# Kernel optimization log

Hardware: AMD Instinct MI355X
Metric: run time of the kernel (lower is better)

The kernel has to match this reference:

```python
import jax, jax.numpy as jnp
import numpy as np
import math

D_MODEL, D_K, N_HEADS = 1024, 64, 16
N, T = 2, 2048


def setup_inputs() -> dict:
    key = jax.random.key(0)
    ks = jax.random.split(key, 12)
    s = 1.0 / math.sqrt(D_MODEL)
    dh = D_K * N_HEADS
    return {
        "k": jax.random.normal(ks[0], (N, T, D_MODEL), jnp.float32),
        "q": jax.random.normal(ks[1], (N, T, D_MODEL), jnp.float32),
        "v": jax.random.normal(ks[2], (N, T, D_MODEL), jnp.float32),
        "mask": jnp.ones((N, T), jnp.int32),
        "Wk": jax.random.normal(ks[3], (D_MODEL, dh), jnp.float32) * s,
        "bk": jnp.zeros((dh,), jnp.float32),
        "Wq": jax.random.normal(ks[4], (D_MODEL, dh), jnp.float32) * s,
        "bq": jnp.zeros((dh,), jnp.float32),
        "Wv": jax.random.normal(ks[5], (D_MODEL, dh), jnp.float32) * s,
        "bv": jnp.zeros((dh,), jnp.float32),
        "Wo": jax.random.normal(ks[6], (dh, D_MODEL), jnp.float32) * (1.0 / math.sqrt(dh)),
        "bo": jnp.zeros((D_MODEL,), jnp.float32),
    }


def reference(k, q, v, mask, Wk, bk, Wq, bq, Wv, bv, Wo, bo):
    n, t = k.shape[0], k.shape[1]
    # project and split heads -> (N, H, T, d_k)
    K = (k @ Wk + bk).reshape(n, t, N_HEADS, D_K).transpose(0, 2, 1, 3)
    Q = (q @ Wq + bq).reshape(n, t, N_HEADS, D_K).transpose(0, 2, 1, 3)
    V = (v @ Wv + bv).reshape(n, t, N_HEADS, D_K).transpose(0, 2, 1, 3)
    scores = jnp.einsum("bhqd,bhkd->bhqk", Q, K) / math.sqrt(D_K)
    scores = jnp.where(mask[:, None, None, :] == 0, -jnp.inf, scores)
    weights = jax.nn.softmax(scores, axis=-1)
    A = jnp.einsum("bhqk,bhkd->bhqd", weights, V)
    A = A.transpose(0, 2, 1, 3).reshape(n, t, N_HEADS * D_K)
    return A @ Wo + bo
```

## Files before the change

### kernel.cpp

```cpp
#include <hip/hip_runtime.h>


typedef __bf16 bf16;
typedef __bf16 bf16x8 __attribute__((ext_vector_type(8)));
typedef __bf16 bf16x4 __attribute__((ext_vector_type(4)));
typedef float f32x4 __attribute__((ext_vector_type(4)));

#define MFMA16(a, b, c) __builtin_amdgcn_mfma_f32_16x16x32_bf16((a), (b), (c), 0, 0, 0)
#define EXP2(x) __builtin_amdgcn_exp2f(x)

__device__ __forceinline__ void load_lds16(const bf16* g, bf16* l) {
  __builtin_amdgcn_global_load_lds(
      (const __attribute__((address_space(1))) unsigned int*)g,
      (__attribute__((address_space(3))) unsigned int*)l, 16, 0, 0);
}

__device__ __forceinline__ bf16x8 cvt8(const float* __restrict__ p) {
  const f32x4 a = *(const f32x4*)p;
  const f32x4 b = *(const f32x4*)(p + 4);
  bf16x8 r;
  r[0] = (bf16)a[0]; r[1] = (bf16)a[1]; r[2] = (bf16)a[2]; r[3] = (bf16)a[3];
  r[4] = (bf16)b[0]; r[5] = (bf16)b[1]; r[6] = (bf16)b[2]; r[7] = (bf16)b[3];
  return r;
}

__global__ __launch_bounds__(256) void prep(
    const float* __restrict__ ka, const float* __restrict__ qa,
    const float* __restrict__ va, bf16* __restrict__ kb,
    bf16* __restrict__ qb, bf16* __restrict__ vb,
    const float* __restrict__ W0, const float* __restrict__ W1,
    const float* __restrict__ W2, const float* __restrict__ W3,
    bf16* __restrict__ T0, bf16* __restrict__ T1, bf16* __restrict__ T2,
    bf16* __restrict__ T3, const int* __restrict__ mask,
    unsigned long long* __restrict__ mbits) {
  __shared__ bf16 t[64 * 72];
  const int tid = threadIdx.x;
  if (blockIdx.x < 6144) {
    const size_t i = ((size_t)blockIdx.x * 256 + tid) * 8;
    const int which = (int)(i >> 22);
    const size_t off = i & ((size_t)(1u << 22) - 1);
    const float* src = which == 0 ? ka : (which == 1 ? qa : va);
    bf16* dst = which == 0 ? kb : (which == 1 ? qb : vb);
    *(bf16x8*)&dst[off] = cvt8(&src[off]);
    return;
  }
  const int tb = blockIdx.x - 6144;
  const int z = tb >> 8;
  const int rem = tb & 255;
  const int by = rem >> 4, bx = rem & 15;
  const float* W = z == 0 ? W0 : (z == 1 ? W1 : (z == 2 ? W2 : W3));
  bf16* T = z == 0 ? T0 : (z == 1 ? T1 : (z == 2 ? T2 : T3));
  const int kBase = by * 64, nBase = bx * 64;
  const int row = tid >> 2, cs = (tid & 3) * 16;

  const float* src = &W[(size_t)(kBase + row) * 1024 + nBase + cs];
  *(bf16x8*)&t[row * 72 + cs] = cvt8(src);
  *(bf16x8*)&t[row * 72 + cs + 8] = cvt8(src + 8);
  __syncthreads();

  const int n = tid >> 2, ks = (tid & 3) * 16;
  bf16 buf[16];
#pragma unroll
  for (int j = 0; j < 16; ++j) buf[j] = t[(ks + j) * 72 + n];
  bf16* dst = &T[(size_t)(nBase + n) * 1024 + kBase + ks];
  *(bf16x8*)&dst[0] = *(bf16x8*)&buf[0];
  *(bf16x8*)&dst[8] = *(bf16x8*)&buf[8];

  if (bx == 0 && by == 0 && tid < 128) {
    const int w = tid >> 6, lane = tid & 63;
#pragma unroll
    for (int i = 0; i < 8; ++i) {
      const int tile = z * 16 + w * 8 + i;
      const unsigned long long bits = __ballot(mask[tile * 64 + lane] != 0);
      if (lane == 0) mbits[tile] = bits;
    }
  }
}

__global__ __launch_bounds__(256) void gemm_qkv(
    const bf16* __restrict__ kb, const bf16* __restrict__ vb,
    const bf16* __restrict__ qb, const bf16* __restrict__ WkT,
    const bf16* __restrict__ WvT, const bf16* __restrict__ WqT,
    const float* __restrict__ bk, const float* __restrict__ bv,
    const float* __restrict__ bq, bf16* __restrict__ K_buf,
    bf16* __restrict__ Vt_buf, bf16* __restrict__ Q_buf) {
  __shared__ __align__(16) bf16 S[12288];
  bf16* As = S;
  bf16* Ws = S + 8192;
  const int tid = threadIdx.x;
  const int lane = tid & 63, w = tid >> 6;
  const int l15 = lane & 15, quad = lane >> 4;
  const int z = blockIdx.z;
  const bf16* X = z == 0 ? kb : (z == 1 ? vb : qb);
  const bf16* WT = z == 0 ? WkT : (z == 1 ? WvT : WqT);
  const float* B = z == 0 ? bk : (z == 1 ? bv : bq);
  const int mBase = blockIdx.y * 128, nBase = blockIdx.x * 64;
  const int wm = (w >> 1) * 64, wn = (w & 1) * 32;

  const int r8 = tid >> 3;
  const int jg = ((tid & 7) ^ (r8 & 7)) * 8;
  const int sw = l15 & 7;

  f32x4 acc[4][2] = {};

  for (int k0 = 0; k0 < 1024; k0 += 64) {
    __syncthreads();
#pragma unroll
    for (int i = 0; i < 4; ++i)
      load_lds16(&X[(size_t)(mBase + r8 + i * 32) * 1024 + k0 + jg],
                 &As[(tid + i * 256) * 8]);
#pragma unroll
    for (int i = 0; i < 2; ++i)
      load_lds16(&WT[(size_t)(nBase + r8 + i * 32) * 1024 + k0 + jg],
                 &Ws[(tid + i * 256) * 8]);
    __syncthreads();

#pragma unroll
    for (int k2 = 0; k2 < 2; ++k2) {
      const int col = ((k2 * 4 + quad) ^ sw) * 8;
      bf16x8 a[4], bb[2];
#pragma unroll
      for (int mt = 0; mt < 4; ++mt)
        a[mt] = *(const bf16x8*)&As[(wm + mt * 16 + l15) * 64 + col];
#pragma unroll
      for (int nt = 0; nt < 2; ++nt)
        bb[nt] = *(const bf16x8*)&Ws[(wn + nt * 16 + l15) * 64 + col];
#pragma unroll
      for (int mt = 0; mt < 4; ++mt)
#pragma unroll
        for (int nt = 0; nt < 2; ++nt)
          acc[mt][nt] = MFMA16(a[mt], bb[nt], acc[mt][nt]);
    }
  }

  const int h = nBase >> 6;
  if (z != 1) {
    const float scale = (z == 2) ? 0.18033688011112042f : 1.0f;
    bf16* o = (z == 0) ? K_buf : Q_buf;
#pragma unroll
    for (int nt = 0; nt < 2; ++nt) {
      const int n = nBase + wn + nt * 16 + l15;
      const float bias = B[n];
      const int d = n & 63;
#pragma unroll
      for (int mt = 0; mt < 4; ++mt)
#pragma unroll
        for (int r = 0; r < 4; ++r) {
          const int m = mBase + wm + mt * 16 + quad * 4 + r;
          const int b = m >> 11, t = m & 2047;
          o[((size_t)(b * 16 + h) * 2048 + t) * 64 + d] =
              (bf16)((acc[mt][nt][r] + bias) * scale);
        }
    }
  } else {
    __syncthreads();
    bf16* Tb = &S[w * 2304];
#pragma unroll
    for (int nt = 0; nt < 2; ++nt) {
      const int n = nBase + wn + nt * 16 + l15;
      const float bias = B[n];
#pragma unroll
      for (int mt = 0; mt < 4; ++mt) {
        bf16x4 pk;
#pragma unroll
        for (int r = 0; r < 4; ++r) pk[r] = (bf16)(acc[mt][nt][r] + bias);
        *(bf16x4*)&Tb[(nt * 16 + l15) * 72 + mt * 16 + quad * 4] = pk;
      }
    }
    const int b = mBase >> 11;
#pragma unroll
    for (int i = 0; i < 4; ++i) {
      const int dl = i * 8 + (lane >> 3), ts = (lane & 7) * 8;
      const bf16x8 vv = *(const bf16x8*)&Tb[dl * 72 + ts];
      const int d = wn + dl;
      const int t = (mBase + wm + ts) & 2047;
      *(bf16x8*)&Vt_buf[((size_t)(b * 16 + h) * 64 + d) * 2048 + t] = vv;
    }
  }
}

__global__ __launch_bounds__(256) void gemm_out(const bf16* __restrict__ X,
                                                const bf16* __restrict__ WT,
                                                const float* __restrict__ B,
                                                float* __restrict__ out) {
  __shared__ __align__(16) bf16 As[128 * 64];
  __shared__ __align__(16) bf16 Ws[64 * 64];
  const int tid = threadIdx.x;
  const int lane = tid & 63, w = tid >> 6;
  const int l15 = lane & 15, quad = lane >> 4;
  const int mBase = blockIdx.y * 128, nBase = blockIdx.x * 64;
  const int wm = (w >> 1) * 64, wn = (w & 1) * 32;

  const int r8 = tid >> 3;
  const int jg = ((tid & 7) ^ (r8 & 7)) * 8;
  const int sw = l15 & 7;

  f32x4 acc[4][2] = {};

  for (int k0 = 0; k0 < 1024; k0 += 64) {
    __syncthreads();
#pragma unroll
    for (int i = 0; i < 4; ++i)
      load_lds16(&X[(size_t)(mBase + r8 + i * 32) * 1024 + k0 + jg],
                 &As[(tid + i * 256) * 8]);
#pragma unroll
    for (int i = 0; i < 2; ++i)
      load_lds16(&WT[(size_t)(nBase + r8 + i * 32) * 1024 + k0 + jg],
                 &Ws[(tid + i * 256) * 8]);
    __syncthreads();

#pragma unroll
    for (int k2 = 0; k2 < 2; ++k2) {
      const int col = ((k2 * 4 + quad) ^ sw) * 8;
      bf16x8 a[4], bb[2];
#pragma unroll
      for (int mt = 0; mt < 4; ++mt)
        a[mt] = *(const bf16x8*)&As[(wm + mt * 16 + l15) * 64 + col];
#pragma unroll
      for (int nt = 0; nt < 2; ++nt)
        bb[nt] = *(const bf16x8*)&Ws[(wn + nt * 16 + l15) * 64 + col];
#pragma unroll
      for (int mt = 0; mt < 4; ++mt)
#pragma unroll
        for (int nt = 0; nt < 2; ++nt)
          acc[mt][nt] = MFMA16(a[mt], bb[nt], acc[mt][nt]);
    }
  }

#pragma unroll
  for (int nt = 0; nt < 2; ++nt) {
    const int n = nBase + wn + nt * 16 + l15;
    const float bias = B[n];
#pragma unroll
    for (int mt = 0; mt < 4; ++mt)
#pragma unroll
      for (int r = 0; r < 4; ++r) {
        const int m = mBase + wm + mt * 16 + quad * 4 + r;
        out[(size_t)m * 1024 + n] = acc[mt][nt][r] + bias;
      }
  }
}

__global__ __launch_bounds__(256) void flash_attn(
    const bf16* __restrict__ Q, const bf16* __restrict__ K,
    const bf16* __restrict__ Vt, const unsigned long long* __restrict__ mbits,
    bf16* __restrict__ A) {
  __shared__ __align__(16) bf16 Ks[2][64 * 64];
  __shared__ __align__(16) bf16 Vs[64 * 64];
  __shared__ __align__(16) bf16 Ps[128 * 72];

  const int tid = threadIdx.x;
  const int lane = tid & 63, w = tid >> 6;
  const int l15 = lane & 15, quad = lane >> 4;
  const int bh = blockIdx.y;
  const int b = bh >> 4, h = bh & 15;
  const int qt = blockIdx.x * 128;

  const int r8 = tid >> 3;
  const int jg = ((tid & 7) ^ (r8 & 7)) * 8;
  const int sw = l15 & 7;

  const size_t qbaseA = ((size_t)bh * 2048 + qt + w * 32 + l15) * 64;
  const size_t qbaseB = qbaseA + (size_t)16 * 64;
  const bf16x8 qA0 = *(const bf16x8*)&Q[qbaseA + quad * 8];
  const bf16x8 qA1 = *(const bf16x8*)&Q[qbaseA + 32 + quad * 8];
  const bf16x8 qB0 = *(const bf16x8*)&Q[qbaseB + quad * 8];
  const bf16x8 qB1 = *(const bf16x8*)&Q[qbaseB + 32 + quad * 8];

  f32x4 oA[4] = {}, oB[4] = {};
  float rsA = 0.0f, rsB = 0.0f;

  const int rowA = (w * 32 + l15) * 72;
  const int rowB = (w * 32 + 16 + l15) * 72;

#pragma unroll
  for (int i = 0; i < 2; ++i)
    load_lds16(&K[((size_t)bh * 2048 + r8 + i * 32) * 64 + jg],
               &Ks[0][(tid + i * 256) * 8]);

  int cur = 0;
  for (int kt = 0; kt < 2048; kt += 64) {
    __builtin_amdgcn_s_barrier();

    const unsigned long long mb = mbits[b * 32 + (kt >> 6)];

#pragma unroll
    for (int i = 0; i < 2; ++i)
      load_lds16(&Vt[((size_t)bh * 64 + r8 + i * 32) * 2048 + kt + jg],
                 &Vs[(tid + i * 256) * 8]);
    const int ktn = (kt + 64) & 2047;
#pragma unroll
    for (int i = 0; i < 2; ++i)
      load_lds16(&K[((size_t)bh * 2048 + ktn + r8 + i * 32) * 64 + jg],
                 &Ks[cur ^ 1][(tid + i * 256) * 8]);

    asm volatile("s_waitcnt vmcnt(4)" ::: "memory");
    __builtin_amdgcn_s_barrier();

    const bf16* Kc = Ks[cur];
    f32x4 sA[4], sB[4];
    __builtin_amdgcn_s_setprio(1);
#pragma unroll
    for (int nt = 0; nt < 4; ++nt) {
      const bf16x8 ak0 = *(const bf16x8*)&Kc[(nt * 16 + l15) * 64 + ((quad ^ sw) * 8)];
      const bf16x8 ak1 = *(const bf16x8*)&Kc[(nt * 16 + l15) * 64 + (((4 + quad) ^ sw) * 8)];
      f32x4 s = {};
      s = MFMA16(ak0, qA0, s);
      s = MFMA16(ak1, qA1, s);
      sA[nt] = s;
      f32x4 t = {};
      t = MFMA16(ak0, qB0, t);
      t = MFMA16(ak1, qB1, t);
      sB[nt] = t;
    }
    __builtin_amdgcn_s_setprio(0);

    asm volatile("s_waitcnt vmcnt(2)" ::: "memory");

    if (mb + 1ull == 0ull) {
#pragma unroll
      for (int nt = 0; nt < 4; ++nt) {
        const float a0 = EXP2(sA[nt][0]), a1 = EXP2(sA[nt][1]);
        const float a2 = EXP2(sA[nt][2]), a3 = EXP2(sA[nt][3]);
        rsA += (a0 + a1) + (a2 + a3);
        bf16x4 pa;
        pa[0] = (bf16)a0; pa[1] = (bf16)a1; pa[2] = (bf16)a2; pa[3] = (bf16)a3;
        *(bf16x4*)&Ps[rowA + nt * 16 + quad * 4] = pa;
        const float b0 = EXP2(sB[nt][0]), b1 = EXP2(sB[nt][1]);
        const float b2 = EXP2(sB[nt][2]), b3 = EXP2(sB[nt][3]);
        rsB += (b0 + b1) + (b2 + b3);
        bf16x4 pb;
        pb[0] = (bf16)b0; pb[1] = (bf16)b1; pb[2] = (bf16)b2; pb[3] = (bf16)b3;
        *(bf16x4*)&Ps[rowB + nt * 16 + quad * 4] = pb;
      }
    } else {
#pragma unroll
      for (int nt = 0; nt < 4; ++nt) {
        const unsigned g = (unsigned)(mb >> (nt * 16)) & 0xffffu;
        const int bp = quad * 4;
        const unsigned m0 = (g >> (bp + 0)) & 1u, m1 = (g >> (bp + 1)) & 1u;
        const unsigned m2 = (g >> (bp + 2)) & 1u, m3 = (g >> (bp + 3)) & 1u;
        const float a0 = m0 ? EXP2(sA[nt][0]) : 0.0f;
        const float a1 = m1 ? EXP2(sA[nt][1]) : 0.0f;
        const float a2 = m2 ? EXP2(sA[nt][2]) : 0.0f;
        const float a3 = m3 ? EXP2(sA[nt][3]) : 0.0f;
        rsA += (a0 + a1) + (a2 + a3);
        bf16x4 pa;
        pa[0] = (bf16)a0; pa[1] = (bf16)a1; pa[2] = (bf16)a2; pa[3] = (bf16)a3;
        *(bf16x4*)&Ps[rowA + nt * 16 + quad * 4] = pa;
        const float b0 = m0 ? EXP2(sB[nt][0]) : 0.0f;
        const float b1 = m1 ? EXP2(sB[nt][1]) : 0.0f;
        const float b2 = m2 ? EXP2(sB[nt][2]) : 0.0f;
        const float b3 = m3 ? EXP2(sB[nt][3]) : 0.0f;
        rsB += (b0 + b1) + (b2 + b3);
        bf16x4 pb;
        pb[0] = (bf16)b0; pb[1] = (bf16)b1; pb[2] = (bf16)b2; pb[3] = (bf16)b3;
        *(bf16x4*)&Ps[rowB + nt * 16 + quad * 4] = pb;
      }
    }

    __builtin_amdgcn_s_barrier();

    __builtin_amdgcn_s_setprio(1);
#pragma unroll
    for (int ks = 0; ks < 2; ++ks) {
      const bf16x8 bpA = *(const bf16x8*)&Ps[rowA + ks * 32 + quad * 8];
      const bf16x8 bpB = *(const bf16x8*)&Ps[rowB + ks * 32 + quad * 8];
#pragma unroll
      for (int mt = 0; mt < 4; ++mt) {
        const bf16x8 av =
            *(const bf16x8*)&Vs[(mt * 16 + l15) * 64 + (((ks * 4 + quad) ^ sw) * 8)];
        oA[mt] = MFMA16(av, bpA, oA[mt]);
        oB[mt] = MFMA16(av, bpB, oB[mt]);
      }
    }
    __builtin_amdgcn_s_setprio(0);

    cur ^= 1;
  }

  rsA += __shfl_xor(rsA, 16);
  rsA += __shfl_xor(rsA, 32);
  rsB += __shfl_xor(rsB, 16);
  rsB += __shfl_xor(rsB, 32);
  const float invA = rsA > 0.0f ? 1.0f / rsA : 0.0f;
  const float invB = rsB > 0.0f ? 1.0f / rsB : 0.0f;

  const int tA = qt + w * 32 + l15;
  const size_t baseA = ((size_t)b * 2048 + tA) * 1024 + h * 64;
  const size_t baseB = baseA + (size_t)16 * 1024;
#pragma unroll
  for (int mt = 0; mt < 4; ++mt) {
    bf16x4 ovA, ovB;
#pragma unroll
    for (int r = 0; r < 4; ++r) {
      ovA[r] = (bf16)(oA[mt][r] * invA);
      ovB[r] = (bf16)(oB[mt][r] * invB);
    }
    *(bf16x4*)&A[baseA + mt * 16 + quad * 4] = ovA;
    *(bf16x4*)&A[baseB + mt * 16 + quad * 4] = ovB;
  }
}

extern "C" void kernel_launch(void* const* d_in, const int* in_sizes, int n_in,
                              void* d_out, int out_size, void* d_ws, size_t ws_size,
                              hipStream_t stream) {
  const float* k = (const float*)d_in[0];
  const float* q = (const float*)d_in[1];
  const float* v = (const float*)d_in[2];
  const int* mask = (const int*)d_in[3];
  const float* Wk = (const float*)d_in[4];
  const float* bk = (const float*)d_in[5];
  const float* Wq = (const float*)d_in[6];
  const float* bq = (const float*)d_in[7];
  const float* Wv = (const float*)d_in[8];
  const float* bv = (const float*)d_in[9];
  const float* Wo = (const float*)d_in[10];
  const float* bo = (const float*)d_in[11];

  const size_t ELEMS = (size_t)4 * 1024 * 1024;
  const size_t WELEMS = (size_t)1024 * 1024;

  bf16* kb = (bf16*)d_ws;
  bf16* qb = kb + ELEMS;
  bf16* vb = qb + ELEMS;
  bf16* WkT = vb + ELEMS;
  bf16* WqT = WkT + WELEMS;
  bf16* WvT = WqT + WELEMS;
  bf16* WoT = WvT + WELEMS;

  bf16 *K_buf, *Q_buf, *Vt_buf, *A_buf;
  if (ws_size >= ((size_t)56 << 20)) {
    bf16* ext = WoT + WELEMS;
    K_buf = ext;
    Q_buf = ext + ELEMS;
    Vt_buf = ext + 2 * ELEMS;
    A_buf = kb;
  } else {
    K_buf = (bf16*)d_in[0];
    Q_buf = (bf16*)d_in[0] + ELEMS;
    Vt_buf = (bf16*)d_in[2];
    A_buf = (bf16*)d_in[2] + ELEMS;
  }
  unsigned long long* mbits = (unsigned long long*)d_out;

  prep<<<7168, 256, 0, stream>>>(k, q, v, kb, qb, vb,
                                 Wk, Wq, Wv, Wo, WkT, WqT, WvT, WoT,
                                 mask, mbits);
  gemm_qkv<<<dim3(16, 32, 3), 256, 0, stream>>>(kb, vb, qb, WkT, WvT, WqT,
                                                bk, bv, bq, K_buf, Vt_buf, Q_buf);
  flash_attn<<<dim3(16, 32), 256, 0, stream>>>(Q_buf, K_buf, Vt_buf, mbits, A_buf);
  gemm_out<<<dim3(16, 32), 256, 0, stream>>>(A_buf, WoT, bo, (float*)d_out);
}
```

Before: 224.7 us.

## Switch attention to 32x32 MFMA and keep P in registers via permlane swap

Rewrites the flash attention inner loop to use 32x32x16 bf16 MFMA tiles for both QK^T and PV. Softmax probabilities are packed with v_cvt_pk_bf16_f32 and rearranged across lane halves with v_permlane32_swap, so they feed the PV MFMA directly instead of going through an LDS round-trip. This drops the Ps shared buffer and its stores and loads, lowers LDS use, and halves the row-sum shuffle work. The cost is more accumulator registers per lane and reliance on gfx950-specific permlane instructions.

After: 243.3 us. 1.08x slower.

```diff
diff --git a/kernel.cpp b/kernel.cpp
--- a/kernel.cpp
+++ b/kernel.cpp
@@ -5,8 +5,11 @@
 typedef __bf16 bf16x8 __attribute__((ext_vector_type(8)));
 typedef __bf16 bf16x4 __attribute__((ext_vector_type(4)));
 typedef float f32x4 __attribute__((ext_vector_type(4)));
+typedef float f32x16 __attribute__((ext_vector_type(16)));
+typedef unsigned u32x4 __attribute__((ext_vector_type(4)));
 
 #define MFMA16(a, b, c) __builtin_amdgcn_mfma_f32_16x16x32_bf16((a), (b), (c), 0, 0, 0)
+#define MFMA32(a, b, c) __builtin_amdgcn_mfma_f32_32x32x16_bf16((a), (b), (c), 0, 0, 0)
 #define EXP2(x) __builtin_amdgcn_exp2f(x)
 
 __device__ __forceinline__ void load_lds16(const bf16* g, bf16* l) {
@@ -247,31 +250,27 @@
     bf16* __restrict__ A) {
   __shared__ __align__(16) bf16 Ks[2][64 * 64];
   __shared__ __align__(16) bf16 Vs[64 * 64];
-  __shared__ __align__(16) bf16 Ps[128 * 72];
 
   const int tid = threadIdx.x;
   const int lane = tid & 63, w = tid >> 6;
-  const int l15 = lane & 15, quad = lane >> 4;
+  const int l31 = lane & 31, hi = lane >> 5;
+  const int m7 = l31 & 7;
   const int bh = blockIdx.y;
   const int b = bh >> 4, h = bh & 15;
   const int qt = blockIdx.x * 128;
 
   const int r8 = tid >> 3;
   const int jg = ((tid & 7) ^ (r8 & 7)) * 8;
-  const int sw = l15 & 7;
-
-  const size_t qbaseA = ((size_t)bh * 2048 + qt + w * 32 + l15) * 64;
-  const size_t qbaseB = qbaseA + (size_t)16 * 64;
-  const bf16x8 qA0 = *(const bf16x8*)&Q[qbaseA + quad * 8];
-  const bf16x8 qA1 = *(const bf16x8*)&Q[qbaseA + 32 + quad * 8];
-  const bf16x8 qB0 = *(const bf16x8*)&Q[qbaseB + quad * 8];
-  const bf16x8 qB1 = *(const bf16x8*)&Q[qbaseB + 32 + quad * 8];
-
-  f32x4 oA[4] = {}, oB[4] = {};
-  float rsA = 0.0f, rsB = 0.0f;
-
-  const int rowA = (w * 32 + l15) * 72;
-  const int rowB = (w * 32 + 16 + l15) * 72;
+
+  const int q = qt + w * 32 + l31;
+  const size_t qbase = ((size_t)bh * 2048 + q) * 64;
+  bf16x8 qf[4];
+#pragma unroll
+  for (int t = 0; t < 4; ++t)
+    qf[t] = *(const bf16x8*)&Q[qbase + t * 16 + hi * 8];
+
+  f32x16 o_acc[2] = {};
+  float rs = 0.0f;
 
 #pragma unroll
   for (int i = 0; i < 2; ++i)
@@ -298,108 +297,100 @@
     __builtin_amdgcn_s_barrier();
 
     const bf16* Kc = Ks[cur];
-    f32x4 sA[4], sB[4];
+    f32x16 s_acc[2];
     __builtin_amdgcn_s_setprio(1);
 #pragma unroll
-    for (int nt = 0; nt < 4; ++nt) {
-      const bf16x8 ak0 = *(const bf16x8*)&Kc[(nt * 16 + l15) * 64 + ((quad ^ sw) * 8)];
-      const bf16x8 ak1 = *(const bf16x8*)&Kc[(nt * 16 + l15) * 64 + (((4 + quad) ^ sw) * 8)];
-      f32x4 s = {};
-      s = MFMA16(ak0, qA0, s);
-      s = MFMA16(ak1, qA1, s);
-      sA[nt] = s;
-      f32x4 t = {};
-      t = MFMA16(ak0, qB0, t);
-      t = MFMA16(ak1, qB1, t);
-      sB[nt] = t;
+    for (int kk = 0; kk < 2; ++kk) {
+      f32x16 s = {};
+#pragma unroll
+      for (int t = 0; t < 4; ++t) {
+        const int row = kk * 32 + l31;
+        const bf16x8 ak =
+            *(const bf16x8*)&Kc[row * 64 + (((2 * t + hi) ^ m7) * 8)];
+        s = MFMA32(ak, qf[t], s);
+      }
+      s_acc[kk] = s;
     }
     __builtin_amdgcn_s_setprio(0);
 
     asm volatile("s_waitcnt vmcnt(2)" ::: "memory");
 
+    unsigned c[2][4][2];
     if (mb + 1ull == 0ull) {
 #pragma unroll
-      for (int nt = 0; nt < 4; ++nt) {
-        const float a0 = EXP2(sA[nt][0]), a1 = EXP2(sA[nt][1]);
-        const float a2 = EXP2(sA[nt][2]), a3 = EXP2(sA[nt][3]);
-        rsA += (a0 + a1) + (a2 + a3);
-        bf16x4 pa;
-        pa[0] = (bf16)a0; pa[1] = (bf16)a1; pa[2] = (bf16)a2; pa[3] = (bf16)a3;
-        *(bf16x4*)&Ps[rowA + nt * 16 + quad * 4] = pa;
-        const float b0 = EXP2(sB[nt][0]), b1 = EXP2(sB[nt][1]);
-        const float b2 = EXP2(sB[nt][2]), b3 = EXP2(sB[nt][3]);
-        rsB += (b0 + b1) + (b2 + b3);
-        bf16x4 pb;
-        pb[0] = (bf16)b0; pb[1] = (bf16)b1; pb[2] = (bf16)b2; pb[3] = (bf16)b3;
-        *(bf16x4*)&Ps[rowB + nt * 16 + quad * 4] = pb;
+      for (int kk = 0; kk < 2; ++kk)
+#pragma unroll
+        for (int sg = 0; sg < 4; ++sg)
+#pragma unroll
+          for (int i = 0; i < 2; ++i) {
+            const float p0 = EXP2(s_acc[kk][sg * 4 + 2 * i]);
+            const float p1 = EXP2(s_acc[kk][sg * 4 + 2 * i + 1]);
+            rs += p0 + p1;
+            unsigned u;
+            asm("v_cvt_pk_bf16_f32 %0, %1, %2" : "=v"(u) : "v"(p0), "v"(p1));
+            c[kk][sg][i] = u;
+          }
+    } else {
+#pragma unroll
+      for (int kk = 0; kk < 2; ++kk) {
+        const unsigned g = (unsigned)(mb >> (kk * 32));
+#pragma unroll
+        for (int sg = 0; sg < 4; ++sg)
+#pragma unroll
+          for (int i = 0; i < 2; ++i) {
+            const int kl = sg * 8 + hi * 4 + 2 * i;
+            const float p0 = ((g >> kl) & 1u) ? EXP2(s_acc[kk][sg * 4 + 2 * i]) : 0.0f;
+            const float p1 = ((g >> (kl + 1)) & 1u) ? EXP2(s_acc[kk][sg * 4 + 2 * i + 1]) : 0.0f;
+            rs += p0 + p1;
+            unsigned u;
+            asm("v_cvt_pk_bf16_f32 %0, %1, %2" : "=v"(u) : "v"(p0), "v"(p1));
+            c[kk][sg][i] = u;
+          }
       }
-    } else {
-#pragma unroll
-      for (int nt = 0; nt < 4; ++nt) {
-        const unsigned g = (unsigned)(mb >> (nt * 16)) & 0xffffu;
-        const int bp = quad * 4;
-        const unsigned m0 = (g >> (bp + 0)) & 1u, m1 = (g >> (bp + 1)) & 1u;
-        const unsigned m2 = (g >> (bp + 2)) & 1u, m3 = (g >> (bp + 3)) & 1u;
-        const float a0 = m0 ? EXP2(sA[nt][0]) : 0.0f;
-        const float a1 = m1 ? EXP2(sA[nt][1]) : 0.0f;
-        const float a2 = m2 ? EXP2(sA[nt][2]) : 0.0f;
-        const float a3 = m3 ? EXP2(sA[nt][3]) : 0.0f;
-        rsA += (a0 + a1) + (a2 + a3);
-        bf16x4 pa;
-        pa[0] = (bf16)a0; pa[1] = (bf16)a1; pa[2] = (bf16)a2; pa[3] = (bf16)a3;
-        *(bf16x4*)&Ps[rowA + nt * 16 + quad * 4] = pa;
-        const float b0 = m0 ? EXP2(sB[nt][0]) : 0.0f;
-        const float b1 = m1 ? EXP2(sB[nt][1]) : 0.0f;
-        const float b2 = m2 ? EXP2(sB[nt][2]) : 0.0f;
-        const float b3 = m3 ? EXP2(sB[nt][3]) : 0.0f;
-        rsB += (b0 + b1) + (b2 + b3);
-        bf16x4 pb;
-        pb[0] = (bf16)b0; pb[1] = (bf16)b1; pb[2] = (bf16)b2; pb[3] = (bf16)b3;
-        *(bf16x4*)&Ps[rowB + nt * 16 + quad * 4] = pb;
+    }
+
+    __builtin_amdgcn_s_barrier();
+
+    const bf16* Vc = Vs;
+    __builtin_amdgcn_s_setprio(1);
+#pragma unroll
+    for (int kk = 0; kk < 2; ++kk)
+#pragma unroll
+      for (int t2 = 0; t2 < 2; ++t2) {
+        unsigned a0 = c[kk][2 * t2][0], b0 = c[kk][2 * t2 + 1][0];
+        asm("v_permlane32_swap_b32 %0, %1" : "+v"(a0), "+v"(b0));
+        unsigned a1 = c[kk][2 * t2][1], b1 = c[kk][2 * t2 + 1][1];
+        asm("v_permlane32_swap_b32 %0, %1" : "+v"(a1), "+v"(b1));
+        u32x4 wv;
+        wv[0] = a0; wv[1] = a1; wv[2] = b0; wv[3] = b1;
+        const bf16x8 bp = __builtin_bit_cast(bf16x8, wv);
+        const int seg = kk * 2 + t2;
+#pragma unroll
+        for (int dt = 0; dt < 2; ++dt) {
+          const int row = dt * 32 + l31;
+          const bf16x8 av =
+              *(const bf16x8*)&Vc[row * 64 + (((seg * 2 + hi) ^ m7) * 8)];
+          o_acc[dt] = MFMA32(av, bp, o_acc[dt]);
+        }
       }
-    }
-
-    __builtin_amdgcn_s_barrier();
-
-    __builtin_amdgcn_s_setprio(1);
-#pragma unroll
-    for (int ks = 0; ks < 2; ++ks) {
-      const bf16x8 bpA = *(const bf16x8*)&Ps[rowA + ks * 32 + quad * 8];
-      const bf16x8 bpB = *(const bf16x8*)&Ps[rowB + ks * 32 + quad * 8];
-#pragma unroll
-      for (int mt = 0; mt < 4; ++mt) {
-        const bf16x8 av =
-            *(const bf16x8*)&Vs[(mt * 16 + l15) * 64 + (((ks * 4 + quad) ^ sw) * 8)];
-        oA[mt] = MFMA16(av, bpA, oA[mt]);
-        oB[mt] = MFMA16(av, bpB, oB[mt]);
-      }
-    }
     __builtin_amdgcn_s_setprio(0);
 
     cur ^= 1;
   }
 
-  rsA += __shfl_xor(rsA, 16);
-  rsA += __shfl_xor(rsA, 32);
-  rsB += __shfl_xor(rsB, 16);
-  rsB += __shfl_xor(rsB, 32);
-  const float invA = rsA > 0.0f ? 1.0f / rsA : 0.0f;
-  const float invB = rsB > 0.0f ? 1.0f / rsB : 0.0f;
-
-  const int tA = qt + w * 32 + l15;
-  const size_t baseA = ((size_t)b * 2048 + tA) * 1024 + h * 64;
-  const size_t baseB = baseA + (size_t)16 * 1024;
-#pragma unroll
-  for (int mt = 0; mt < 4; ++mt) {
-    bf16x4 ovA, ovB;
-#pragma unroll
-    for (int r = 0; r < 4; ++r) {
-      ovA[r] = (bf16)(oA[mt][r] * invA);
-      ovB[r] = (bf16)(oB[mt][r] * invB);
-    }
-    *(bf16x4*)&A[baseA + mt * 16 + quad * 4] = ovA;
-    *(bf16x4*)&A[baseB + mt * 16 + quad * 4] = ovB;
-  }
+  rs += __shfl_xor(rs, 32);
+  const float inv = rs > 0.0f ? 1.0f / rs : 0.0f;
+
+  const size_t base = ((size_t)b * 2048 + q) * 1024 + h * 64;
+#pragma unroll
+  for (int dt = 0; dt < 2; ++dt)
+#pragma unroll
+    for (int rg = 0; rg < 4; ++rg) {
+      bf16x4 ov;
+#pragma unroll
+      for (int r = 0; r < 4; ++r) ov[r] = (bf16)(o_acc[dt][rg * 4 + r] * inv);
+      *(bf16x4*)&A[base + dt * 32 + rg * 8 + hi * 4] = ov;
+    }
 }
 
 extern "C" void kernel_launch(void* const* d_in, const int* in_sizes, int n_in,
```
